# Kernel optimization log

Measured on AMD Instinct MI355X. Metric: run time of the kernel, lower is better.

## Reference

```python
import jax, jax.numpy as jnp
import numpy as np

SIGMA = 0.1
EPS = 1e-12

def setup_inputs() -> dict:
    key = jax.random.key(0)
    emb_org = jax.random.normal(key, (8192, 256), dtype=jnp.float32)
    return {"emb_org": emb_org}

def reference(emb_org):
    # L2-normalize rows (clamp norm at 1e-12 like torch)
    norm = jnp.clip(jnp.linalg.norm(emb_org, axis=1, keepdims=True), EPS, None)
    emb_n = emb_org / norm                      # [N, D]
    W = jnp.matmul(emb_n, emb_n.T) / SIGMA      # [N, N] cosine sim / sigma
    T = jax.nn.softmax(W, axis=1)               # row softmax
    emb_sft = jnp.matmul(T, emb_org)            # [N, D]
    return emb_sft
```

## Files before the change

kernel.cpp:

```cpp
#include <hip/hip_runtime.h>
#include <hip/hip_bf16.h>
#include <stdint.h>

#define NROWS 8192
#define DDIM  256
#define SIGMA_INV 10.0f

#define BM 64
#define BN 64
#define NSPLIT 4
#define JCHUNK (NROWS / NSPLIT)
#define NITER  (JCHUNK / BN)
#define PSTR   72
#define KCHB   1056

typedef __attribute__((ext_vector_type(8))) short bf16x8;
typedef __attribute__((ext_vector_type(4))) float f32x4;

__device__ inline unsigned short f2bf(float x) {
  __hip_bfloat16 h = __float2bfloat16(x);
  return *reinterpret_cast<unsigned short*>(&h);
}

__device__ inline void dma16(const void* g, void* l) {
  __builtin_amdgcn_global_load_lds(
      (const __attribute__((address_space(1))) unsigned int*)g,
      (__attribute__((address_space(3))) unsigned int*)l, 16, 0, 0);
}

__global__ __launch_bounds__(256) void normalize_k(const float* __restrict__ emb,
                                                   unsigned short* __restrict__ embn) {
  const int w = threadIdx.x >> 6, lane = threadIdx.x & 63;
  const int row = blockIdx.x * 4 + w;
  const float4* src = (const float4*)(emb + (size_t)row * DDIM);
  float4 v = src[lane];
  float ss = v.x * v.x + v.y * v.y + v.z * v.z + v.w * v.w;
  for (int off = 32; off >= 1; off >>= 1) ss += __shfl_xor(ss, off);
  const float sc = 1.0f / fmaxf(sqrtf(ss), 1e-12f);
  ushort4 o;
  o.x = f2bf(v.x * sc); o.y = f2bf(v.y * sc);
  o.z = f2bf(v.z * sc); o.w = f2bf(v.w * sc);
  ((ushort4*)(embn + (size_t)row * DDIM))[lane] = o;
}

__global__ __launch_bounds__(256) void transpose_k(const float* __restrict__ emb,
                                                   unsigned short* __restrict__ vt) {
  __shared__ float tile[64][65];
  const int r0 = blockIdx.x * 64, c0 = blockIdx.y * 64;
  const int tr = threadIdx.x >> 6, tc = threadIdx.x & 63;
  for (int i = 0; i < 16; ++i)
    tile[i * 4 + tr][tc] = emb[(size_t)(r0 + i * 4 + tr) * DDIM + c0 + tc];
  __syncthreads();
  for (int i = 0; i < 16; ++i)
    vt[(size_t)(c0 + i * 4 + tr) * NROWS + r0 + tc] = f2bf(tile[tc][i * 4 + tr]);
}

__global__ __launch_bounds__(256, 2) void fused_k(
    const unsigned short* __restrict__ embn,
    const unsigned short* __restrict__ vt,
    float* __restrict__ out,
    float* __restrict__ l_part)
{
  __shared__ char kn[32 * KCHB];
  __shared__ unsigned short pl[BM * PSTR];

  const int tid = threadIdx.x;
  const int w = tid >> 6, lane = tid & 63;
  const int mg = w >> 1, dh = w & 1;
  const int q = lane >> 4, c = lane & 15;
  const int chunk = blockIdx.x & 3;
  const int mblk = blockIdx.x >> 2;
  const int row0 = mblk * BM + mg * 32;
  const size_t j0base = (size_t)chunk * JCHUNK;

  bf16x8 qa[2][8];
  for (int mt = 0; mt < 2; ++mt)
    for (int k = 0; k < 8; ++k)
      qa[mt][k] = *(const bf16x8*)(embn + (size_t)(row0 + mt * 16 + c) * DDIM + k * 32 + q * 8);

  f32x4 oacc[2][8];
  for (int mt = 0; mt < 2; ++mt)
    for (int u = 0; u < 8; ++u) oacc[mt][u] = {0.f, 0.f, 0.f, 0.f};
  float lacc[2][4] = {};

  {
    const char* src = (const char*)(embn + j0base * DDIM);
    for (int cc = 0; cc < 8; ++cc) {
      const int ch = w * 8 + cc;
      dma16(src + ch * 1024 + lane * 16, kn + ch * KCHB + lane * 16);
    }
  }

  for (int it = 0; it < NITER; ++it) {
    const size_t j0 = j0base + (size_t)it * BN;
    __syncthreads();

    f32x4 sacc[2][2];
    for (int mt = 0; mt < 2; ++mt)
      for (int nt = 0; nt < 2; ++nt) sacc[mt][nt] = {0.f, 0.f, 0.f, 0.f};
    const int rb0 = (dh * 16 + (c >> 1)) * KCHB + (c & 1) * 512;
    const int rb1 = (dh * 16 + 8 + (c >> 1)) * KCHB + (c & 1) * 512;
    for (int k = 0; k < 8; ++k) {
      bf16x8 b0 = *(const bf16x8*)(kn + rb0 + k * 64 + q * 16);
      bf16x8 b1 = *(const bf16x8*)(kn + rb1 + k * 64 + q * 16);
      for (int mt = 0; mt < 2; ++mt) {
        sacc[mt][0] = __builtin_amdgcn_mfma_f32_16x16x32_bf16(qa[mt][k], b0, sacc[mt][0], 0, 0, 0);
        sacc[mt][1] = __builtin_amdgcn_mfma_f32_16x16x32_bf16(qa[mt][k], b1, sacc[mt][1], 0, 0, 0);
      }
    }

    bf16x8 vfrag[2][8];
    for (int kk = 0; kk < 2; ++kk)
      for (int u = 0; u < 8; ++u) {
        const int d = dh * 128 + u * 16 + c;
        vfrag[kk][u] = *(const bf16x8*)(vt + (size_t)d * NROWS + j0 + kk * 32 + q * 8);
      }

    for (int mt = 0; mt < 2; ++mt)
      for (int nt = 0; nt < 2; ++nt)
        for (int r = 0; r < 4; ++r) {
          const float p = __expf(fmaf(SIGMA_INV, sacc[mt][nt][r], -SIGMA_INV));
          lacc[mt][r] += p;
          pl[(mg * 32 + mt * 16 + q * 4 + r) * PSTR + dh * 32 + nt * 16 + c] = f2bf(p);
        }

    __syncthreads();

    for (int kk = 0; kk < 2; ++kk) {
      bf16x8 ap0 = *(const bf16x8*)(pl + (mg * 32 + c) * PSTR + kk * 32 + q * 8);
      bf16x8 ap1 = *(const bf16x8*)(pl + (mg * 32 + 16 + c) * PSTR + kk * 32 + q * 8);
      for (int u = 0; u < 8; ++u) {
        oacc[0][u] = __builtin_amdgcn_mfma_f32_16x16x32_bf16(ap0, vfrag[kk][u], oacc[0][u], 0, 0, 0);
        oacc[1][u] = __builtin_amdgcn_mfma_f32_16x16x32_bf16(ap1, vfrag[kk][u], oacc[1][u], 0, 0, 0);
      }
    }

    if (it + 1 < NITER) {
      const char* src = (const char*)(embn + (j0base + (size_t)(it + 1) * BN) * DDIM);
      for (int cc = 0; cc < 8; ++cc) {
        const int ch = w * 8 + cc;
        dma16(src + ch * 1024 + lane * 16, kn + ch * KCHB + lane * 16);
      }
    }
  }

  for (int mt = 0; mt < 2; ++mt)
    for (int r = 0; r < 4; ++r) {
      float s = lacc[mt][r];
      s += __shfl_xor(s, 1); s += __shfl_xor(s, 2);
      s += __shfl_xor(s, 4); s += __shfl_xor(s, 8);
      if (c == 0)
        atomicAdd(&l_part[row0 + mt * 16 + q * 4 + r], s);
    }
  for (int mt = 0; mt < 2; ++mt)
    for (int u = 0; u < 8; ++u)
      for (int r = 0; r < 4; ++r)
        atomicAdd(&out[(size_t)(row0 + mt * 16 + q * 4 + r) * DDIM + dh * 128 + u * 16 + c],
                  oacc[mt][u][r]);
}

__global__ __launch_bounds__(256) void finalize_k(float* __restrict__ out,
                                                  const float* __restrict__ l_part) {
  const int row = blockIdx.x, t = threadIdx.x;
  out[(size_t)row * DDIM + t] /= l_part[row];
}

extern "C" void kernel_launch(void* const* d_in, const int* in_sizes, int n_in,
                              void* d_out, int out_size, void* d_ws, size_t ws_size,
                              hipStream_t stream) {
  const float* emb = (const float*)d_in[0];
  float* out = (float*)d_out;
  char* ws = (char*)d_ws;
  unsigned short* embn = (unsigned short*)ws;
  unsigned short* vt   = (unsigned short*)(ws + ((size_t)4 << 20));
  float* l_part        = (float*)(ws + ((size_t)8 << 20));

  hipMemsetAsync(out, 0, (size_t)NROWS * DDIM * sizeof(float), stream);
  hipMemsetAsync(l_part, 0, (size_t)NROWS * sizeof(float), stream);

  normalize_k<<<NROWS / 4, 256, 0, stream>>>(emb, embn);
  transpose_k<<<dim3(NROWS / 64, DDIM / 64), 256, 0, stream>>>(emb, vt);
  fused_k<<<(NROWS / BM) * NSPLIT, 256, 0, stream>>>(embn, vt, out, l_part);
  finalize_k<<<NROWS, 256, 0, stream>>>(out, l_part);
}
```

Baseline: 237.4 us.

## Double-buffer K tiles, hoist V loads, and merge prep kernels with zeroing

Gives the fused attention kernel a second LDS buffer for key tiles, so the next tile's async DMA is issued at the top of each iteration and overlaps the current compute. V fragment global loads are also moved before the score MFMAs to hide their latency. Normalization, transpose and the output/l_part memsets are merged into one prep kernel, removing two memset calls and one launch. The extra K buffer roughly doubles that LDS footprint and may lower occupancy, and the V loads now stay live in registers longer.

```diff
diff --git a/kernel.cpp b/kernel.cpp
--- a/kernel.cpp
+++ b/kernel.cpp
@@ -13,6 +13,7 @@
 #define NITER  (JCHUNK / BN)
 #define PSTR   72
 #define KCHB   1056
+#define TPITCH 257
 
 typedef __attribute__((ext_vector_type(8))) short bf16x8;
 typedef __attribute__((ext_vector_type(4))) float f32x4;
@@ -28,31 +29,50 @@
       (__attribute__((address_space(3))) unsigned int*)l, 16, 0, 0);
 }
 
-__global__ __launch_bounds__(256) void normalize_k(const float* __restrict__ emb,
-                                                   unsigned short* __restrict__ embn) {
-  const int w = threadIdx.x >> 6, lane = threadIdx.x & 63;
-  const int row = blockIdx.x * 4 + w;
-  const float4* src = (const float4*)(emb + (size_t)row * DDIM);
-  float4 v = src[lane];
-  float ss = v.x * v.x + v.y * v.y + v.z * v.z + v.w * v.w;
-  for (int off = 32; off >= 1; off >>= 1) ss += __shfl_xor(ss, off);
-  const float sc = 1.0f / fmaxf(sqrtf(ss), 1e-12f);
-  ushort4 o;
-  o.x = f2bf(v.x * sc); o.y = f2bf(v.y * sc);
-  o.z = f2bf(v.z * sc); o.w = f2bf(v.w * sc);
-  ((ushort4*)(embn + (size_t)row * DDIM))[lane] = o;
-}
-
-__global__ __launch_bounds__(256) void transpose_k(const float* __restrict__ emb,
-                                                   unsigned short* __restrict__ vt) {
-  __shared__ float tile[64][65];
-  const int r0 = blockIdx.x * 64, c0 = blockIdx.y * 64;
-  const int tr = threadIdx.x >> 6, tc = threadIdx.x & 63;
-  for (int i = 0; i < 16; ++i)
-    tile[i * 4 + tr][tc] = emb[(size_t)(r0 + i * 4 + tr) * DDIM + c0 + tc];
+__global__ __launch_bounds__(256) void prep_k(const float* __restrict__ emb,
+                                              unsigned short* __restrict__ embn,
+                                              unsigned short* __restrict__ vt,
+                                              float* __restrict__ out,
+                                              float* __restrict__ l_part) {
+  __shared__ float tile[64 * TPITCH];
+  __shared__ float nrm[64];
+  const int t = threadIdx.x, tr = t >> 6, tc = t & 63;
+  const int row0 = blockIdx.x * 64;
+
+  {
+    float4 z = {0.f, 0.f, 0.f, 0.f};
+    float4* op = (float4*)(out + (size_t)blockIdx.x * 16384);
+    for (int i = 0; i < 16; ++i) op[i * 256 + t] = z;
+    if (blockIdx.x < 32) l_part[blockIdx.x * 256 + t] = 0.f;
+  }
+
+  for (int i = 0; i < 16; ++i) {
+    const int r = i * 4 + tr;
+    float4 v = *(const float4*)(emb + (size_t)(row0 + r) * DDIM + tc * 4);
+    tile[r * TPITCH + tc * 4 + 0] = v.x;
+    tile[r * TPITCH + tc * 4 + 1] = v.y;
+    tile[r * TPITCH + tc * 4 + 2] = v.z;
+    tile[r * TPITCH + tc * 4 + 3] = v.w;
+    float ss = v.x * v.x + v.y * v.y + v.z * v.z + v.w * v.w;
+    for (int off = 32; off >= 1; off >>= 1) ss += __shfl_xor(ss, off);
+    if (tc == 0) nrm[r] = 1.0f / fmaxf(sqrtf(ss), 1e-12f);
+  }
   __syncthreads();
-  for (int i = 0; i < 16; ++i)
-    vt[(size_t)(c0 + i * 4 + tr) * NROWS + r0 + tc] = f2bf(tile[tc][i * 4 + tr]);
+
+  for (int i = 0; i < 16; ++i) {
+    const int r = i * 4 + tr;
+    const float sc = nrm[r];
+    ushort4 o;
+    o.x = f2bf(tile[r * TPITCH + tc * 4 + 0] * sc);
+    o.y = f2bf(tile[r * TPITCH + tc * 4 + 1] * sc);
+    o.z = f2bf(tile[r * TPITCH + tc * 4 + 2] * sc);
+    o.w = f2bf(tile[r * TPITCH + tc * 4 + 3] * sc);
+    ((ushort4*)(embn + (size_t)(row0 + r) * DDIM))[tc] = o;
+  }
+  for (int i = 0; i < 64; ++i) {
+    const int d = i * 4 + tr;
+    vt[(size_t)d * NROWS + row0 + tc] = f2bf(tile[tc * TPITCH + d]);
+  }
 }
 
 __global__ __launch_bounds__(256, 2) void fused_k(
@@ -61,7 +81,7 @@
     float* __restrict__ out,
     float* __restrict__ l_part)
 {
-  __shared__ char kn[32 * KCHB];
+  __shared__ char kn[2][32 * KCHB];
   __shared__ unsigned short pl[BM * PSTR];
 
   const int tid = threadIdx.x;
@@ -87,13 +107,29 @@
     const char* src = (const char*)(embn + j0base * DDIM);
     for (int cc = 0; cc < 8; ++cc) {
       const int ch = w * 8 + cc;
-      dma16(src + ch * 1024 + lane * 16, kn + ch * KCHB + lane * 16);
+      dma16(src + ch * 1024 + lane * 16, kn[0] + ch * KCHB + lane * 16);
     }
   }
 
   for (int it = 0; it < NITER; ++it) {
+    const int buf = it & 1;
     const size_t j0 = j0base + (size_t)it * BN;
     __syncthreads();
+
+    if (it + 1 < NITER) {
+      const char* src = (const char*)(embn + (j0 + BN) * DDIM);
+      for (int cc = 0; cc < 8; ++cc) {
+        const int ch = w * 8 + cc;
+        dma16(src + ch * 1024 + lane * 16, kn[buf ^ 1] + ch * KCHB + lane * 16);
+      }
+    }
+
+    bf16x8 vfrag[2][8];
+    for (int kk = 0; kk < 2; ++kk)
+      for (int u = 0; u < 8; ++u) {
+        const int d = dh * 128 + u * 16 + c;
+        vfrag[kk][u] = *(const bf16x8*)(vt + (size_t)d * NROWS + j0 + kk * 32 + q * 8);
+      }
 
     f32x4 sacc[2][2];
     for (int mt = 0; mt < 2; ++mt)
@@ -101,20 +137,13 @@
     const int rb0 = (dh * 16 + (c >> 1)) * KCHB + (c & 1) * 512;
     const int rb1 = (dh * 16 + 8 + (c >> 1)) * KCHB + (c & 1) * 512;
     for (int k = 0; k < 8; ++k) {
-      bf16x8 b0 = *(const bf16x8*)(kn + rb0 + k * 64 + q * 16);
-      bf16x8 b1 = *(const bf16x8*)(kn + rb1 + k * 64 + q * 16);
+      bf16x8 b0 = *(const bf16x8*)(kn[buf] + rb0 + k * 64 + q * 16);
+      bf16x8 b1 = *(const bf16x8*)(kn[buf] + rb1 + k * 64 + q * 16);
       for (int mt = 0; mt < 2; ++mt) {
         sacc[mt][0] = __builtin_amdgcn_mfma_f32_16x16x32_bf16(qa[mt][k], b0, sacc[mt][0], 0, 0, 0);
         sacc[mt][1] = __builtin_amdgcn_mfma_f32_16x16x32_bf16(qa[mt][k], b1, sacc[mt][1], 0, 0, 0);
       }
     }
-
-    bf16x8 vfrag[2][8];
-    for (int kk = 0; kk < 2; ++kk)
-      for (int u = 0; u < 8; ++u) {
-        const int d = dh * 128 + u * 16 + c;
-        vfrag[kk][u] = *(const bf16x8*)(vt + (size_t)d * NROWS + j0 + kk * 32 + q * 8);
-      }
 
     for (int mt = 0; mt < 2; ++mt)
       for (int nt = 0; nt < 2; ++nt)
@@ -132,14 +161,6 @@
       for (int u = 0; u < 8; ++u) {
         oacc[0][u] = __builtin_amdgcn_mfma_f32_16x16x32_bf16(ap0, vfrag[kk][u], oacc[0][u], 0, 0, 0);
         oacc[1][u] = __builtin_amdgcn_mfma_f32_16x16x32_bf16(ap1, vfrag[kk][u], oacc[1][u], 0, 0, 0);
-      }
-    }
-
-    if (it + 1 < NITER) {
-      const char* src = (const char*)(embn + (j0base + (size_t)(it + 1) * BN) * DDIM);
-      for (int cc = 0; cc < 8; ++cc) {
-        const int ch = w * 8 + cc;
-        dma16(src + ch * 1024 + lane * 16, kn + ch * KCHB + lane * 16);
       }
     }
   }
@@ -175,11 +196,7 @@
   unsigned short* vt   = (unsigned short*)(ws + ((size_t)4 << 20));
   float* l_part        = (float*)(ws + ((size_t)8 << 20));
 
-  hipMemsetAsync(out, 0, (size_t)NROWS * DDIM * sizeof(float), stream);
-  hipMemsetAsync(l_part, 0, (size_t)NROWS * sizeof(float), stream);
-
-  normalize_k<<<NROWS / 4, 256, 0, stream>>>(emb, embn);
-  transpose_k<<<dim3(NROWS / 64, DDIM / 64), 256, 0, stream>>>(emb, vt);
+  prep_k<<<NROWS / 64, 256, 0, stream>>>(emb, embn, vt, out, l_part);
   fused_k<<<(NROWS / BM) * NSPLIT, 256, 0, stream>>>(embn, vt, out, l_part);
   finalize_k<<<NROWS, 256, 0, stream>>>(out, l_part);
 }
```

Measured after the change: 239.9 us. Within noise of the previous version (+1.1%).
